# Performance work log

Hardware: AMD Instinct MI355X
Metric: run time of the kernel (lower is better)

The kernel has to match this reference:

```python
import jax, jax.numpy as jnp
import numpy as np

C_IN = 256
C_INNER = C_IN // 8  # reduction=8 -> 32


def setup_inputs() -> dict:
    key = jax.random.key(0)
    ks = jax.random.split(key, 10)
    s = 0.05
    return {
        "x": jax.random.normal(ks[0], (8, C_IN, 64, 64), dtype=jnp.float32),
        "w_theta": jax.random.normal(ks[1], (C_INNER, C_IN), dtype=jnp.float32) * s,
        "b_theta": jnp.zeros((C_INNER,), dtype=jnp.float32),
        "w_phi": jax.random.normal(ks[2], (C_INNER, C_IN), dtype=jnp.float32) * s,
        "b_phi": jnp.zeros((C_INNER,), dtype=jnp.float32),
        "w_g": jax.random.normal(ks[3], (C_INNER, C_IN), dtype=jnp.float32) * s,
        "b_g": jnp.zeros((C_INNER,), dtype=jnp.float32),
        "w_attn": jax.random.normal(ks[4], (C_IN, C_INNER), dtype=jnp.float32) * s,
        "b_attn": jnp.zeros((C_IN,), dtype=jnp.float32),
        "sigma": jnp.zeros((1,), dtype=jnp.float32),
    }


def _proj(x, w, bias):
    # 1x1 conv: x [b,c,h,w], w [k,c] -> [b,k,h,w]
    return jnp.einsum('bchw,kc->bkhw', x, w) + bias[None, :, None, None]


def reference(x, w_theta, b_theta, w_phi, b_phi, w_g, b_g, w_attn, b_attn, sigma):
    b, c, h, w = x.shape
    n = h * w
    theta = _proj(x, w_theta, b_theta).reshape(b, -1, n)  # [b,k,n]
    phi = _proj(x, w_phi, b_phi).reshape(b, -1, n)        # [b,k,n]
    g = _proj(x, w_g, b_g).reshape(b, -1, n)              # [b,k,n]
    # attn[b, i, j] = softmax_j( theta[:, :, i] . phi[:, :, j] )
    attn = jax.nn.softmax(jnp.einsum('bki,bkj->bij', theta, phi), axis=-1)
    # attn_g[b, k, i] = sum_j g[b,k,j] * attn[b,i,j]
    attn_g = jnp.einsum('bkj,bij->bki', g, attn).reshape(b, -1, h, w)
    out_proj = _proj(attn_g, w_attn, b_attn)
    return x + sigma * out_proj
```

## Files before the change

### kernel.cpp

```cpp
#include <hip/hip_runtime.h>
#include <hip/hip_bf16.h>


using f32x4  = __attribute__((ext_vector_type(4))) float;
using bf16x8 = __attribute__((ext_vector_type(8))) short;

#define NB   8
#define CIN  256
#define KD   32
#define NN   4096

#define Q_OFF    0
#define K_OFF    (NB * NN * KD)
#define VT_OFF   (2 * NB * NN * KD)
#define WB_OFF   (VT_OFF + NB * KD * NN)
#define WAB_OFF  (WB_OFF + 96 * 256)
#define WS_ELEMS (WAB_OFF + 256 * 32)

__device__ __forceinline__ short f2bf(float f) {
    unsigned u = __builtin_bit_cast(unsigned, f);
    u += 0x7fffu + ((u >> 16) & 1u);
    return (short)(u >> 16);
}

__device__ __forceinline__ unsigned pack_bf2(float a, float b) {
    return (unsigned)(unsigned short)f2bf(a) |
           ((unsigned)(unsigned short)f2bf(b) << 16);
}

__global__ __launch_bounds__(256) void prep_kernel(
    const float* __restrict__ wt, const float* __restrict__ wp,
    const float* __restrict__ wg, const float* __restrict__ wa,
    short* __restrict__ ws)
{
    int t = blockIdx.x * 256 + threadIdx.x;
    if (t < 96 * 256) {
        float v = (t < 32 * 256) ? wt[t]
                : (t < 64 * 256) ? wp[t - 32 * 256]
                                 : wg[t - 64 * 256];
        ws[WB_OFF + t] = f2bf(v);
    } else {
        int t2 = t - 96 * 256;
        ws[WAB_OFF + t2] = f2bf(wa[t2]);
    }
}

#define CSTR 264

__global__ __launch_bounds__(256, 4) void proj_kernel(
    const float* __restrict__ x,
    const float* __restrict__ bt, const float* __restrict__ bp,
    const float* __restrict__ bg,
    short* __restrict__ ws)
{
    __shared__ __attribute__((aligned(16))) short xT[64 * CSTR];
    __shared__ __attribute__((aligned(16))) short vtl[KD * 72];

    const int blk = blockIdx.x;
    const int b   = blk & 7;
    const int n0  = (blk >> 3) * 64;
    const int tid = threadIdx.x;

    {
        const int nq = (tid & 15) * 4;
        const int cb = tid >> 4;
        #pragma unroll
        for (int pass = 0; pass < 2; ++pass) {
            float4 v[8];
            #pragma unroll
            for (int u = 0; u < 8; ++u) {
                const int c = pass * 128 + u * 16 + cb;
                v[u] = *reinterpret_cast<const float4*>(
                    x + (size_t)(b * CIN + c) * NN + n0 + nq);
            }
            #pragma unroll
            for (int u = 0; u < 8; ++u) {
                const int c = pass * 128 + u * 16 + cb;
                xT[(nq + 0) * CSTR + c] = f2bf(v[u].x);
                xT[(nq + 1) * CSTR + c] = f2bf(v[u].y);
                xT[(nq + 2) * CSTR + c] = f2bf(v[u].z);
                xT[(nq + 3) * CSTR + c] = f2bf(v[u].w);
            }
        }
    }
    __syncthreads();

    const int lane = tid & 63;
    const int wv   = tid >> 6;
    const int cL   = lane & 15;
    const int g    = lane >> 4;

    f32x4 acc[6];
    #pragma unroll
    for (int kt = 0; kt < 6; ++kt) acc[kt] = f32x4{0.f, 0.f, 0.f, 0.f};

    const short* Wb = ws + WB_OFF;
    #pragma unroll
    for (int kc = 0; kc < 8; ++kc) {
        bf16x8 a = *reinterpret_cast<const bf16x8*>(
            &xT[(wv * 16 + cL) * CSTR + kc * 32 + g * 8]);
        #pragma unroll
        for (int kt = 0; kt < 6; ++kt) {
            bf16x8 bb = *reinterpret_cast<const bf16x8*>(
                Wb + (kt * 16 + cL) * 256 + kc * 32 + g * 8);
            acc[kt] = __builtin_amdgcn_mfma_f32_16x16x32_bf16(a, bb, acc[kt], 0, 0, 0);
        }
    }

    #pragma unroll
    for (int kt = 0; kt < 4; ++kt) {
        const float bias = (kt < 2) ? bt[kt * 16 + cL] : bp[(kt - 2) * 16 + cL];
        #pragma unroll
        for (int r = 0; r < 4; ++r) {
            xT[(wv * 16 + 4 * g + r) * CSTR + kt * 16 + cL] =
                f2bf(acc[kt][r] + bias);
        }
    }
    #pragma unroll
    for (int kt = 4; kt < 6; ++kt) {
        const float bias = bg[(kt - 4) * 16 + cL];
        const int d = (kt - 4) * 16 + cL;
        unsigned lo = pack_bf2(acc[kt][0] + bias, acc[kt][1] + bias);
        unsigned hi = pack_bf2(acc[kt][2] + bias, acc[kt][3] + bias);
        *reinterpret_cast<uint2*>(&vtl[d * 72 + wv * 16 + 4 * g]) = make_uint2(lo, hi);
    }
    __syncthreads();

    {
        short* Qd = ws + Q_OFF;
        short* Kd = ws + K_OFF;
        const int row  = tid >> 2;
        const int slot = tid & 3;
        uint4 qv = *reinterpret_cast<const uint4*>(&xT[row * CSTR + slot * 8]);
        uint4 kv = *reinterpret_cast<const uint4*>(&xT[row * CSTR + 32 + slot * 8]);
        *reinterpret_cast<uint4*>(Qd + (size_t)(b * NN + n0 + row) * KD + slot * 8) = qv;
        *reinterpret_cast<uint4*>(Kd + (size_t)(b * NN + n0 + row) * KD + slot * 8) = kv;

        short* VT = ws + VT_OFF;
        const int d  = tid >> 3;
        const int nn = (tid & 7) * 8;
        bf16x8 v = *reinterpret_cast<const bf16x8*>(&vtl[d * 72 + nn]);
        *reinterpret_cast<bf16x8*>(&VT[(size_t)(b * KD + d) * NN + n0 + nn]) = v;
    }
}

#define JT    128
#define NT    (NN / JT)
#define KSTR  40
#define VSTR  136
#define PSTR  72
#define OSTR  40

#define KT0_  0
#define KT1_  (JT * KSTR)
#define VT0_  (2 * JT * KSTR)
#define VT1_  (VT0_ + KD * VSTR)
#define P_    (VT0_ + 2 * KD * VSTR)
#define LDS_SZ (P_ + 8 * 16 * PSTR)

__global__ __launch_bounds__(512, 2) void attn_kernel(
    const float* __restrict__ x,
    const float* __restrict__ ba,
    const float* __restrict__ sigma_p,
    const short* __restrict__ ws,
    float* __restrict__ out)
{
    __shared__ __attribute__((aligned(16))) short lds[LDS_SZ];

    const int blk  = blockIdx.x;
    const int b    = blk & 7;
    const int i0   = (blk >> 3) * 128;
    const int tid  = threadIdx.x;
    const int wv   = tid >> 6;
    const int lane = tid & 63;
    const int cL   = lane & 15;
    const int g    = lane >> 4;

    const short* Qd = ws + Q_OFF  + (size_t)b * NN * KD;
    const short* Kg = ws + K_OFF  + (size_t)b * NN * KD;
    const short* Vg = ws + VT_OFF + (size_t)b * KD * NN;
    short* Pw = lds + P_ + wv * 16 * PSTR;

    const int iw = i0 + wv * 16;
    bf16x8 qf = *reinterpret_cast<const bf16x8*>(Qd + (size_t)(iw + cL) * KD + g * 8);

    const int krow = tid >> 2,  kslot = tid & 3;
    const int vrow = tid >> 4,  vslot = tid & 15;

    const f32x4 zero = f32x4{0.f, 0.f, 0.f, 0.f};
    f32x4 o0 = zero, o1 = zero;
    float lsum = 0.f;

    uint4 kreg = *reinterpret_cast<const uint4*>(
        Kg + (size_t)krow * KD + kslot * 8);
    uint4 vreg = *reinterpret_cast<const uint4*>(
        Vg + (size_t)vrow * NN + vslot * 8);
    *reinterpret_cast<uint4*>(lds + KT0_ + krow * KSTR + kslot * 8) = kreg;
    *reinterpret_cast<uint4*>(lds + VT0_ + vrow * VSTR + vslot * 8) = vreg;
    __syncthreads();

    for (int t = 0; t < NT; ++t) {
        const int cur = t & 1;
        if (t + 1 < NT) {
            kreg = *reinterpret_cast<const uint4*>(
                Kg + (size_t)((t + 1) * JT + krow) * KD + kslot * 8);
            vreg = *reinterpret_cast<const uint4*>(
                Vg + (size_t)vrow * NN + (t + 1) * JT + vslot * 8);
        }
        const short* Kc = lds + (cur ? KT1_ : KT0_);
        const short* Vc = lds + (cur ? VT1_ : VT0_);

        #pragma unroll
        for (int h2 = 0; h2 < 2; ++h2) {
            const int jl = h2 * 64;
            f32x4 s[4];
            #pragma unroll
            for (int jf = 0; jf < 4; ++jf) {
                bf16x8 kf = *reinterpret_cast<const bf16x8*>(
                    Kc + (jl + jf * 16 + cL) * KSTR + g * 8);
                s[jf] = __builtin_amdgcn_mfma_f32_16x16x32_bf16(kf, qf, zero, 0, 0, 0);
            }
            #pragma unroll
            for (int jf = 0; jf < 4; ++jf) {
                float p0 = __expf(s[jf][0]);
                float p1 = __expf(s[jf][1]);
                float p2 = __expf(s[jf][2]);
                float p3 = __expf(s[jf][3]);
                lsum += (p0 + p1) + (p2 + p3);
                unsigned lo = pack_bf2(p0, p1);
                unsigned hi = pack_bf2(p2, p3);
                *reinterpret_cast<uint2*>(Pw + cL * PSTR + jf * 16 + 4 * g) =
                    make_uint2(lo, hi);
            }
            #pragma unroll
            for (int jc = 0; jc < 2; ++jc) {
                bf16x8 pa = *reinterpret_cast<const bf16x8*>(
                    Pw + cL * PSTR + jc * 32 + g * 8);
                bf16x8 v0 = *reinterpret_cast<const bf16x8*>(
                    Vc + (0 + cL) * VSTR + jl + jc * 32 + g * 8);
                bf16x8 v1 = *reinterpret_cast<const bf16x8*>(
                    Vc + (16 + cL) * VSTR + jl + jc * 32 + g * 8);
                o0 = __builtin_amdgcn_mfma_f32_16x16x32_bf16(pa, v0, o0, 0, 0, 0);
                o1 = __builtin_amdgcn_mfma_f32_16x16x32_bf16(pa, v1, o1, 0, 0, 0);
            }
        }

        if (t + 1 < NT) {
            *reinterpret_cast<uint4*>(
                lds + (cur ? KT0_ : KT1_) + krow * KSTR + kslot * 8) = kreg;
            *reinterpret_cast<uint4*>(
                lds + (cur ? VT0_ : VT1_) + vrow * VSTR + vslot * 8) = vreg;
            __syncthreads();
        }
    }

    lsum += __shfl_xor(lsum, 16, 64);
    lsum += __shfl_xor(lsum, 32, 64);
    float rlv[4];
    #pragma unroll
    for (int r = 0; r < 4; ++r) rlv[r] = 1.0f / __shfl(lsum, 4 * g + r, 64);

    short* Ow = lds + wv * 16 * OSTR;
    #pragma unroll
    for (int r = 0; r < 4; ++r) {
        Ow[(4 * g + r) * OSTR +  0 + cL] = f2bf(o0[r] * rlv[r]);
        Ow[(4 * g + r) * OSTR + 16 + cL] = f2bf(o1[r] * rlv[r]);
    }
    bf16x8 ob = *reinterpret_cast<const bf16x8*>(Ow + cL * OSTR + g * 8);

    const float sig = sigma_p[0];
    const short* Wab = ws + WAB_OFF;
    const int nidx = iw + cL;
    #pragma unroll 4
    for (int ct = 0; ct < 16; ++ct) {
        bf16x8 wf = *reinterpret_cast<const bf16x8*>(
            Wab + (ct * 16 + cL) * KD + g * 8);
        f32x4 d = __builtin_amdgcn_mfma_f32_16x16x32_bf16(wf, ob, zero, 0, 0, 0);
        #pragma unroll
        for (int r = 0; r < 4; ++r) {
            const int c = ct * 16 + 4 * g + r;
            const size_t idx = (size_t)(b * CIN + c) * NN + nidx;
            out[idx] = x[idx] + sig * (d[r] + ba[c]);
        }
    }
}

extern "C" void kernel_launch(void* const* d_in, const int* in_sizes, int n_in,
                              void* d_out, int out_size, void* d_ws, size_t ws_size,
                              hipStream_t stream)
{
    const float* x  = (const float*)d_in[0];
    const float* wt = (const float*)d_in[1];
    const float* bt = (const float*)d_in[2];
    const float* wp = (const float*)d_in[3];
    const float* bp = (const float*)d_in[4];
    const float* wg = (const float*)d_in[5];
    const float* bg = (const float*)d_in[6];
    const float* wa = (const float*)d_in[7];
    const float* ba = (const float*)d_in[8];
    const float* sg = (const float*)d_in[9];
    short* ws  = (short*)d_ws;
    float* out = (float*)d_out;

    if (ws_size < (size_t)WS_ELEMS * sizeof(short)) return;

    hipLaunchKernelGGL(prep_kernel, dim3(128), dim3(256), 0, stream,
                       wt, wp, wg, wa, ws);
    hipLaunchKernelGGL(proj_kernel, dim3(512), dim3(256), 0, stream,
                       x, bt, bp, bg, ws);
    hipLaunchKernelGGL(attn_kernel, dim3(256), dim3(512), 0, stream,
                       x, ba, sg, ws, out);
}
```

Measured before the change: 158.8 us.

## Split key range across wave pairs, halve query tile, use exp2 with pre-scaled Q

The attention kernel now gives each block 64 query rows instead of 128, with each pair of waves splitting every 128-key tile into two 64-key halves. This doubles the grid to 512 blocks and raises the occupancy hint. Partial outputs and row sums are combined through LDS before the output projection, which is now split across waves by channel. Q is pre-scaled by log2(e) so the kernel can use the hardware exp2, and P is packed to bf16 by truncation rather than rounding. The cost is extra LDS traffic, more barriers and slightly lower precision in P.

After: 152.7 us. -3.9%, faster.

```diff
diff --git a/kernel.cpp b/kernel.cpp
--- a/kernel.cpp
+++ b/kernel.cpp
@@ -9,6 +9,9 @@
 #define CIN  256
 #define KD   32
 #define NN   4096
+#define LOG2E 1.44269504088896340736f
+
+#define EXP2F(v) __builtin_amdgcn_exp2f(v)
 
 #define Q_OFF    0
 #define K_OFF    (NB * NN * KD)
@@ -26,6 +29,11 @@
 __device__ __forceinline__ unsigned pack_bf2(float a, float b) {
     return (unsigned)(unsigned short)f2bf(a) |
            ((unsigned)(unsigned short)f2bf(b) << 16);
+}
+
+__device__ __forceinline__ unsigned pack_bf2_tr(float a, float b) {
+    return (__builtin_bit_cast(unsigned, b) & 0xffff0000u) |
+           (__builtin_bit_cast(unsigned, a) >> 16);
 }
 
 __global__ __launch_bounds__(256) void prep_kernel(
@@ -110,10 +118,11 @@
     #pragma unroll
     for (int kt = 0; kt < 4; ++kt) {
         const float bias = (kt < 2) ? bt[kt * 16 + cL] : bp[(kt - 2) * 16 + cL];
+        const float sc   = (kt < 2) ? LOG2E : 1.0f;
         #pragma unroll
         for (int r = 0; r < 4; ++r) {
             xT[(wv * 16 + 4 * g + r) * CSTR + kt * 16 + cL] =
-                f2bf(acc[kt][r] + bias);
+                f2bf((acc[kt][r] + bias) * sc);
         }
     }
     #pragma unroll
@@ -150,6 +159,7 @@
 #define VSTR  136
 #define PSTR  72
 #define OSTR  40
+#define OPSTR 33
 
 #define KT0_  0
 #define KT1_  (JT * KSTR)
@@ -157,8 +167,11 @@
 #define VT1_  (VT0_ + KD * VSTR)
 #define P_    (VT0_ + 2 * KD * VSTR)
 #define LDS_SZ (P_ + 8 * 16 * PSTR)
-
-__global__ __launch_bounds__(512, 2) void attn_kernel(
+#define OW_A  0
+#define OP_A  2560
+#define LP_A  (2560 + 8448)
+
+__global__ __launch_bounds__(512, 4) void attn_kernel(
     const float* __restrict__ x,
     const float* __restrict__ ba,
     const float* __restrict__ sigma_p,
@@ -169,19 +182,22 @@
 
     const int blk  = blockIdx.x;
     const int b    = blk & 7;
-    const int i0   = (blk >> 3) * 128;
+    const int i0   = (blk >> 3) * 64;
     const int tid  = threadIdx.x;
     const int wv   = tid >> 6;
     const int lane = tid & 63;
     const int cL   = lane & 15;
     const int g    = lane >> 4;
+    const int rg   = wv >> 1;
+    const int jh   = wv & 1;
+    const int jl   = jh * 64;
 
     const short* Qd = ws + Q_OFF  + (size_t)b * NN * KD;
     const short* Kg = ws + K_OFF  + (size_t)b * NN * KD;
     const short* Vg = ws + VT_OFF + (size_t)b * KD * NN;
     short* Pw = lds + P_ + wv * 16 * PSTR;
 
-    const int iw = i0 + wv * 16;
+    const int iw = i0 + rg * 16;
     bf16x8 qf = *reinterpret_cast<const bf16x8*>(Qd + (size_t)(iw + cL) * KD + g * 8);
 
     const int krow = tid >> 2,  kslot = tid & 3;
@@ -210,39 +226,33 @@
         const short* Kc = lds + (cur ? KT1_ : KT0_);
         const short* Vc = lds + (cur ? VT1_ : VT0_);
 
-        #pragma unroll
-        for (int h2 = 0; h2 < 2; ++h2) {
-            const int jl = h2 * 64;
-            f32x4 s[4];
-            #pragma unroll
-            for (int jf = 0; jf < 4; ++jf) {
-                bf16x8 kf = *reinterpret_cast<const bf16x8*>(
-                    Kc + (jl + jf * 16 + cL) * KSTR + g * 8);
-                s[jf] = __builtin_amdgcn_mfma_f32_16x16x32_bf16(kf, qf, zero, 0, 0, 0);
-            }
-            #pragma unroll
-            for (int jf = 0; jf < 4; ++jf) {
-                float p0 = __expf(s[jf][0]);
-                float p1 = __expf(s[jf][1]);
-                float p2 = __expf(s[jf][2]);
-                float p3 = __expf(s[jf][3]);
-                lsum += (p0 + p1) + (p2 + p3);
-                unsigned lo = pack_bf2(p0, p1);
-                unsigned hi = pack_bf2(p2, p3);
-                *reinterpret_cast<uint2*>(Pw + cL * PSTR + jf * 16 + 4 * g) =
-                    make_uint2(lo, hi);
-            }
-            #pragma unroll
-            for (int jc = 0; jc < 2; ++jc) {
-                bf16x8 pa = *reinterpret_cast<const bf16x8*>(
-                    Pw + cL * PSTR + jc * 32 + g * 8);
-                bf16x8 v0 = *reinterpret_cast<const bf16x8*>(
-                    Vc + (0 + cL) * VSTR + jl + jc * 32 + g * 8);
-                bf16x8 v1 = *reinterpret_cast<const bf16x8*>(
-                    Vc + (16 + cL) * VSTR + jl + jc * 32 + g * 8);
-                o0 = __builtin_amdgcn_mfma_f32_16x16x32_bf16(pa, v0, o0, 0, 0, 0);
-                o1 = __builtin_amdgcn_mfma_f32_16x16x32_bf16(pa, v1, o1, 0, 0, 0);
-            }
+        f32x4 s[4];
+        #pragma unroll
+        for (int jf = 0; jf < 4; ++jf) {
+            bf16x8 kf = *reinterpret_cast<const bf16x8*>(
+                Kc + (jl + jf * 16 + cL) * KSTR + g * 8);
+            s[jf] = __builtin_amdgcn_mfma_f32_16x16x32_bf16(kf, qf, zero, 0, 0, 0);
+        }
+        #pragma unroll
+        for (int jf = 0; jf < 4; ++jf) {
+            float p0 = EXP2F(s[jf][0]);
+            float p1 = EXP2F(s[jf][1]);
+            float p2 = EXP2F(s[jf][2]);
+            float p3 = EXP2F(s[jf][3]);
+            lsum += (p0 + p1) + (p2 + p3);
+            *reinterpret_cast<uint2*>(Pw + cL * PSTR + jf * 16 + 4 * g) =
+                make_uint2(pack_bf2_tr(p0, p1), pack_bf2_tr(p2, p3));
+        }
+        #pragma unroll
+        for (int jc = 0; jc < 2; ++jc) {
+            bf16x8 pa = *reinterpret_cast<const bf16x8*>(
+                Pw + cL * PSTR + jc * 32 + g * 8);
+            bf16x8 v0 = *reinterpret_cast<const bf16x8*>(
+                Vc + (0 + cL) * VSTR + jl + jc * 32 + g * 8);
+            bf16x8 v1 = *reinterpret_cast<const bf16x8*>(
+                Vc + (16 + cL) * VSTR + jl + jc * 32 + g * 8);
+            o0 = __builtin_amdgcn_mfma_f32_16x16x32_bf16(pa, v0, o0, 0, 0, 0);
+            o1 = __builtin_amdgcn_mfma_f32_16x16x32_bf16(pa, v1, o1, 0, 0, 0);
         }
 
         if (t + 1 < NT) {
@@ -253,26 +263,51 @@
             __syncthreads();
         }
     }
+    __syncthreads();
 
     lsum += __shfl_xor(lsum, 16, 64);
     lsum += __shfl_xor(lsum, 32, 64);
-    float rlv[4];
-    #pragma unroll
-    for (int r = 0; r < 4; ++r) rlv[r] = 1.0f / __shfl(lsum, 4 * g + r, 64);
-
-    short* Ow = lds + wv * 16 * OSTR;
-    #pragma unroll
-    for (int r = 0; r < 4; ++r) {
-        Ow[(4 * g + r) * OSTR +  0 + cL] = f2bf(o0[r] * rlv[r]);
-        Ow[(4 * g + r) * OSTR + 16 + cL] = f2bf(o1[r] * rlv[r]);
-    }
-    bf16x8 ob = *reinterpret_cast<const bf16x8*>(Ow + cL * OSTR + g * 8);
+    {
+        float* lp = reinterpret_cast<float*>(lds + LP_A);
+        if (g == 0) lp[wv * 16 + cL] = lsum;
+        float* op = reinterpret_cast<float*>(lds + OP_A) + wv * 16 * OPSTR;
+        #pragma unroll
+        for (int r = 0; r < 4; ++r) {
+            op[(4 * g + r) * OPSTR +  0 + cL] = o0[r];
+            op[(4 * g + r) * OPSTR + 16 + cL] = o1[r];
+        }
+    }
+    __syncthreads();
+
+    {
+        const int r   = tid >> 3;
+        const int dg  = tid & 7;
+        const int rgg = r >> 4, il = r & 15;
+        const float* opA = reinterpret_cast<const float*>(lds + OP_A)
+                         + (rgg * 2) * 16 * OPSTR + il * OPSTR;
+        const float* opB = opA + 16 * OPSTR;
+        const float* lp  = reinterpret_cast<const float*>(lds + LP_A);
+        const float rl = 1.0f / (lp[rgg * 32 + il] + lp[rgg * 32 + 16 + il]);
+        #pragma unroll
+        for (int k = 0; k < 2; ++k) {
+            const int d = dg * 4 + k * 2;
+            float a = (opA[d]     + opB[d]    ) * rl;
+            float c = (opA[d + 1] + opB[d + 1]) * rl;
+            *reinterpret_cast<unsigned*>(lds + OW_A + r * OSTR + d) = pack_bf2(a, c);
+        }
+    }
+    __syncthreads();
 
     const float sig = sigma_p[0];
     const short* Wab = ws + WAB_OFF;
-    const int nidx = iw + cL;
-    #pragma unroll 4
-    for (int ct = 0; ct < 16; ++ct) {
+    const int h  = wv & 3;
+    const int qc = wv >> 2;
+    bf16x8 ob = *reinterpret_cast<const bf16x8*>(
+        lds + OW_A + (h * 16 + cL) * OSTR + g * 8);
+    const int nidx = i0 + h * 16 + cL;
+    #pragma unroll
+    for (int cc = 0; cc < 8; ++cc) {
+        const int ct = qc * 8 + cc;
         bf16x8 wf = *reinterpret_cast<const bf16x8*>(
             Wab + (ct * 16 + cL) * KD + g * 8);
         f32x4 d = __builtin_amdgcn_mfma_f32_16x16x32_bf16(wf, ob, zero, 0, 0, 0);
@@ -304,10 +339,10 @@
 
     if (ws_size < (size_t)WS_ELEMS * sizeof(short)) return;
 
-    hipLaunchKernelGGL(prep_kernel, dim3(128), dim3(256), 0, stream,
+    hipLaunchKernelGGL(prep_kernel, dim3(128),  dim3(256), 0, stream,
                        wt, wp, wg, wa, ws);
-    hipLaunchKernelGGL(proj_kernel, dim3(512), dim3(256), 0, stream,
+    hipLaunchKernelGGL(proj_kernel, dim3(512),  dim3(256), 0, stream,
                        x, bt, bp, bg, ws);
-    hipLaunchKernelGGL(attn_kernel, dim3(256), dim3(512), 0, stream,
+    hipLaunchKernelGGL(attn_kernel, dim3(512),  dim3(512), 0, stream,
                        x, ba, sg, ws, out);
 }
```
